# Kernel tuning notes

Measured on AMD Instinct MI355X. Metric: run time of the kernel, lower is better.

Reference implementation:

```python
import jax, jax.numpy as jnp
import numpy as np

DIM_TIME = 100
NUM_HEAD = 8
DIM_OUT = 256
LN_EPS = 1e-5

# fixed (non-trainable) TimeEncode frequencies: 1 / 10**linspace(0, 9, dim)
_TIME_W = jnp.asarray((1.0 / 10 ** np.linspace(0, 9, DIM_TIME, dtype=np.float32)))


def setup_inputs() -> dict:
    key = jax.random.key(0)
    ks = jax.random.split(key, 16)
    D, E, S = 25000, 500000, 525000
    dn, de = 128, 128
    def lin(k, out_d, in_d):
        return jax.random.normal(k, (out_d, in_d), jnp.float32) * (1.0 / np.sqrt(in_d))
    return {
        "h": jax.random.normal(ks[0], (S, dn), jnp.float32),
        "f": jax.random.normal(ks[1], (E, de), jnp.float32),
        "dt": jax.random.uniform(ks[2], (E,), jnp.float32) * 1000.0,
        "Wq_lin": lin(ks[3], DIM_OUT, dn + DIM_TIME),
        "bq_lin": jnp.zeros((DIM_OUT,), jnp.float32),
        "Wkv_lin": lin(ks[4], DIM_OUT, dn + de + DIM_TIME),
        "bkv_lin": jnp.zeros((DIM_OUT,), jnp.float32),
        "Wq": lin(ks[5], DIM_OUT, DIM_OUT),
        "bq": jnp.zeros((DIM_OUT,), jnp.float32),
        "Wk": lin(ks[6], DIM_OUT, DIM_OUT),
        "bk": jnp.zeros((DIM_OUT,), jnp.float32),
        "Wv": lin(ks[7], DIM_OUT, DIM_OUT),
        "bv": jnp.zeros((DIM_OUT,), jnp.float32),
        "ln_g": jnp.ones((DIM_OUT,), jnp.float32),
        "ln_b": jnp.zeros((DIM_OUT,), jnp.float32),
        "dst": jax.random.randint(ks[8], (E,), 0, D, jnp.int64 if jax.config.jax_enable_x64 else jnp.int32),
    }


def reference(h, f, dt, Wq_lin, bq_lin, Wkv_lin, bkv_lin, Wq, bq, Wk, bk, Wv, bv, ln_g, ln_b, dst):
    E = dst.shape[0]
    D = h.shape[0] - E          # num_dst_nodes; src node D+i is the source of edge i
    H = NUM_HEAD
    dh = DIM_OUT // H

    # TimeEncode (frozen, no grad in original): cos(w * t + 0)
    time_feat = jax.lax.stop_gradient(jnp.cos(dt[:, None] * _TIME_W[None, :]))      # [E, Dt]
    zero_time_feat = jnp.ones((D, DIM_TIME), h.dtype)                               # cos(0) = 1

    # Q from dst nodes; K/V from src-neighbor nodes + edge feat + time feat
    Q_ori = jnp.concatenate([h[:D], zero_time_feat], axis=1) @ Wq_lin.T + bq_lin    # [D, dout]
    K_ori = jnp.concatenate([h[D:], f, time_feat], axis=1) @ Wkv_lin.T + bkv_lin    # [E, dout]

    # augmented edge set: E real edges + D self-loops (dst attends to itself)
    Qfull = jnp.concatenate([Q_ori[dst], Q_ori], axis=0)                            # [E+D, dout]
    KVfull = jnp.concatenate([K_ori, Q_ori], axis=0)                                # [E+D, dout]

    Qh = (Qfull @ Wq.T + bq).reshape(-1, H, dh)
    Kh = (KVfull @ Wk.T + bk).reshape(-1, H, dh)
    Vh = (KVfull @ Wv.T + bv).reshape(-1, H, dh)

    scores = jax.nn.leaky_relu(jnp.sum(Qh * Kh, axis=2), negative_slope=0.2)        # [E+D, H]

    dst_all = jnp.concatenate([dst, jnp.arange(D, dtype=dst.dtype)], axis=0)        # [E+D]

    # segment (edge) softmax over destination nodes; every dst has a self-loop
    seg_max = jnp.full((D, H), -jnp.inf, scores.dtype).at[dst_all].max(scores)
    ex = jnp.exp(scores - seg_max[dst_all])
    seg_sum = jnp.zeros((D, H), scores.dtype).at[dst_all].add(ex)
    att = ex / seg_sum[dst_all]                                                     # [E+D, H]

    # weighted scatter-sum aggregation (copy_u/sum over the augmented block)
    Vw = (Vh * att[:, :, None]).reshape(-1, DIM_OUT)                                # [E+D, dout]
    agg = jnp.zeros((D, DIM_OUT), h.dtype).at[dst_all].add(Vw)                      # [D, dout]

    rst = jax.nn.relu(agg)                                                          # dropout = identity (eval)
    mu = jnp.mean(rst, axis=-1, keepdims=True)
    var = jnp.mean((rst - mu) ** 2, axis=-1, keepdims=True)
    return (rst - mu) * jax.lax.rsqrt(var + LN_EPS) * ln_g + ln_b
```

## Files before the change

kernel.cpp:

```cpp
#include <hip/hip_runtime.h>
#include <cstdint>
#include <cstddef>


typedef _Float16 f16_t;
typedef _Float16 f16x8 __attribute__((ext_vector_type(8)));
typedef _Float16 f16x4 __attribute__((ext_vector_type(4)));
typedef float    f32x4 __attribute__((ext_vector_type(4)));

#define MFMA16(a, b, c) __builtin_amdgcn_mfma_f32_16x16x32_f16(a, b, c, 0, 0, 0)

#define BARRIER()                                         \
  do {                                                    \
    asm volatile("s_waitcnt lgkmcnt(0)" ::: "memory");    \
    __builtin_amdgcn_sched_barrier(0);                    \
    __builtin_amdgcn_s_barrier();                         \
    __builtin_amdgcn_sched_barrier(0);                    \
  } while (0)

static __device__ __forceinline__ f32x4 zero4() {
  f32x4 v; v[0] = 0.f; v[1] = 0.f; v[2] = 0.f; v[3] = 0.f; return v;
}

#define TIMEW_LOG2 (-0.30199346317157837f)

__global__ void k_prep(const float* __restrict__ wq_lin,
                       const float* __restrict__ bq_lin,
                       const float* __restrict__ wq,
                       const float* __restrict__ wk,
                       const float* __restrict__ wv,
                       f16_t* __restrict__ wq1,
                       f16_t* __restrict__ w3,
                       float* __restrict__ bqe) {
  int i = blockIdx.x * 256 + threadIdx.x;
  if (i < 32768) {
    int o = i >> 7, k = i & 127;
    wq1[i] = (f16_t)wq_lin[o * 228 + k];
  } else if (i < 229376) {
    int j = i - 32768;
    int r = j >> 8, k = j & 255;
    const float* src = (r < 256) ? wq : ((r < 512) ? wk : wv);
    w3[j] = (f16_t)src[(r & 255) * 256 + k];
  } else if (i < 229632) {
    int o = i - 229376;
    float s = bq_lin[o];
    for (int j = 0; j < 100; ++j) s += wq_lin[o * 228 + 128 + j];
    bqe[o] = s;
  }
}

__global__ __launch_bounds__(384) void k_wcomp(
    const float* __restrict__ wkv_lin, const float* __restrict__ bkv,
    const float* __restrict__ wk, const float* __restrict__ bk,
    const float* __restrict__ wv, const float* __restrict__ bv,
    f16_t* __restrict__ weffp, float* __restrict__ beff) {
  __shared__ float wrow[256];
  const int oc = blockIdx.x;
  const float* src = (oc < 256) ? (wk + (size_t)oc * 256)
                                : (wv + (size_t)(oc - 256) * 256);
  const int t = threadIdx.x;
  if (t < 256) wrow[t] = src[t];
  __syncthreads();

  float acc = 0.f;
  if (t < 356) {
#pragma unroll 4
    for (int m = 0; m < 256; ++m) acc += wrow[m] * wkv_lin[(size_t)m * 356 + t];
  }
  int kc = t >> 5, g = (t >> 3) & 3, j = t & 7;
  weffp[(size_t)kc * 16384 + g * 4096 + oc * 8 + j] = (f16_t)acc;

  if (t == 0) {
    float b = (oc < 256) ? bk[oc] : bv[oc - 256];
    for (int m = 0; m < 256; ++m) b += wrow[m] * bkv[m];
    beff[oc] = b;
  }
}

__global__ void k_hist(const int* __restrict__ dst, int* __restrict__ rs, int E) {
  int e = blockIdx.x * 256 + threadIdx.x;
  if (e < E) atomicAdd(&rs[dst[e] + 1], 1);
}

__global__ void k_scan(int* __restrict__ rs, int* __restrict__ cur, int D) {
  __shared__ int sd[1024];
  __shared__ int srun;
  const int t = threadIdx.x;
  if (t == 0) srun = 0;
  __syncthreads();
  for (int base = 0; base < D; base += 1024) {
    const int i = base + t;
    int c = (i < D) ? rs[i + 1] : 0;
    sd[t] = c;
    __syncthreads();
    for (int off = 1; off < 1024; off <<= 1) {
      int v = (t >= off) ? sd[t - off] : 0;
      __syncthreads();
      sd[t] += v;
      __syncthreads();
    }
    const int incl = sd[t];
    const int run = srun;
    __syncthreads();
    if (i < D) {
      cur[i] = run + incl - c;
      rs[i + 1] = run + incl;
    }
    if (t == 1023) srun = run + sd[1023];
    __syncthreads();
  }
}

__global__ void k_scatter(const int* __restrict__ dst, int* __restrict__ cur,
                          int* __restrict__ csr, int* __restrict__ dstc, int E) {
  int e = blockIdx.x * 256 + threadIdx.x;
  if (e < E) {
    int d = dst[e];
    int pos = atomicAdd(&cur[d], 1);
    csr[pos] = e;
    dstc[pos] = d;
  }
}

__global__ void k_sentinel(float* __restrict__ o, int n) {
  int i = blockIdx.x * 256 + threadIdx.x;
  if (i < n) o[i] = 1e30f;
}

__global__ __launch_bounds__(512) void k_q(
    const float* __restrict__ h, const float* __restrict__ bqe,
    const float* __restrict__ bq, const float* __restrict__ bk,
    const float* __restrict__ bv, const f16_t* __restrict__ wq1,
    const f16_t* __restrict__ w3, float* __restrict__ qhd,
    f16_t* __restrict__ khs, f16_t* __restrict__ vhs, int D) {
  __shared__ f16_t sm[64 * 256];
  f16_t* xs = sm;
  f16_t* ks = sm;
  const int tid = threadIdx.x;
  const int dbase = blockIdx.x * 64;

  {
    const int r = tid >> 3, q = tid & 7;
    const int dd = min(dbase + r, D - 1);
    const int sw = r & 7;
    const float* p = h + (size_t)dd * 128 + q * 16;
#pragma unroll
    for (int u = 0; u < 2; ++u) {
      float4 v0 = *(const float4*)(p + u * 8);
      float4 v1 = *(const float4*)(p + u * 8 + 4);
      f16x8 w8;
      w8[0] = (f16_t)v0.x; w8[1] = (f16_t)v0.y; w8[2] = (f16_t)v0.z; w8[3] = (f16_t)v0.w;
      w8[4] = (f16_t)v1.x; w8[5] = (f16_t)v1.y; w8[6] = (f16_t)v1.z; w8[7] = (f16_t)v1.w;
      *(f16x8*)&xs[r * 128 + (((2 * q + u) ^ sw) << 3)] = w8;
    }
  }
  __syncthreads();

  const int lane = tid & 63;
  const int wv_ = tid >> 6;
  const int m16 = lane & 15;
  const int g = lane >> 4;

  f32x4 acc1[4][2];
#pragma unroll
  for (int mt = 0; mt < 4; ++mt)
#pragma unroll
    for (int nt = 0; nt < 2; ++nt) acc1[mt][nt] = zero4();

#pragma unroll
  for (int kt = 0; kt < 4; ++kt) {
    f16x8 a[4];
#pragma unroll
    for (int mt = 0; mt < 4; ++mt) {
      int row = mt * 16 + m16;
      a[mt] = *(const f16x8*)&xs[row * 128 + ((((kt << 2) + g) ^ (row & 7)) << 3)];
    }
#pragma unroll
    for (int nt = 0; nt < 2; ++nt) {
      int col = wv_ * 32 + nt * 16 + m16;
      f16x8 b = *(const f16x8*)&wq1[(size_t)col * 128 + (kt << 5) + (g << 3)];
#pragma unroll
      for (int mt = 0; mt < 4; ++mt) acc1[mt][nt] = MFMA16(a[mt], b, acc1[mt][nt]);
    }
  }
  __syncthreads();

#pragma unroll
  for (int nt = 0; nt < 2; ++nt) {
    int col = wv_ * 32 + nt * 16 + m16;
    float bias = bqe[col];
#pragma unroll
    for (int mt = 0; mt < 4; ++mt)
#pragma unroll
      for (int j = 0; j < 4; ++j) {
        int row = mt * 16 + (g << 2) + j;
        ks[row * 256 + ((((col >> 3) ^ (row & 7)) << 3)) + (col & 7)] =
            (f16_t)(acc1[mt][nt][j] + bias);
      }
  }
  __syncthreads();

#pragma unroll
  for (int p = 0; p < 3; ++p) {
    const f16_t* wsec = w3 + ((size_t)p << 16);
    const float* bsec = (p == 0) ? bq : ((p == 1) ? bk : bv);
    f32x4 acc[4][2];
#pragma unroll
    for (int mt = 0; mt < 4; ++mt)
#pragma unroll
      for (int nt = 0; nt < 2; ++nt) acc[mt][nt] = zero4();
#pragma unroll
    for (int kt = 0; kt < 8; ++kt) {
      f16x8 a[4];
#pragma unroll
      for (int mt = 0; mt < 4; ++mt) {
        int row = mt * 16 + m16;
        a[mt] = *(const f16x8*)&ks[row * 256 + ((((kt << 2) + g) ^ (row & 7)) << 3)];
      }
#pragma unroll
      for (int nt = 0; nt < 2; ++nt) {
        int col = wv_ * 32 + nt * 16 + m16;
        f16x8 b = *(const f16x8*)&wsec[(size_t)col * 256 + (kt << 5) + (g << 3)];
#pragma unroll
        for (int mt = 0; mt < 4; ++mt) acc[mt][nt] = MFMA16(a[mt], b, acc[mt][nt]);
      }
    }
#pragma unroll
    for (int nt = 0; nt < 2; ++nt) {
      int col = wv_ * 32 + nt * 16 + m16;
      float bias = bsec[col];
#pragma unroll
      for (int mt = 0; mt < 4; ++mt)
#pragma unroll
        for (int j = 0; j < 4; ++j) {
          int row = mt * 16 + (g << 2) + j;
          int dd = dbase + row;
          if (dd < D) {
            float val = acc[mt][nt][j] + bias;
            if (p == 0)
              qhd[(size_t)dd * 256 + col] = val;
            else if (p == 1)
              khs[(size_t)dd * 256 + col] = (f16_t)val;
            else
              vhs[(size_t)dd * 256 + col] = (f16_t)val;
          }
        }
    }
  }
}

__global__ __launch_bounds__(512, 4) void k_kv(
    const float* __restrict__ h, const float* __restrict__ f,
    const float* __restrict__ dt, const f16_t* __restrict__ weffp,
    const float* __restrict__ beff, const int* __restrict__ csr,
    const int* __restrict__ dstc, const float* __restrict__ qhd,
    float* __restrict__ agg, int D, int E) {
  __shared__ __align__(16) unsigned char smem[40960];

  const int tid = threadIdx.x;
  const int pbase = blockIdx.x * 64;
  const int row = tid >> 3, q = tid & 7;
  const int lane = tid & 63, wn = tid >> 6;
  const int m16 = lane & 15, g = lane >> 4;

  const int pclamp = min(pbase + row, E - 1);
  const int ec = csr[pclamp];
  const float dtv = dt[ec];
  const float* hrow = h + (size_t)(D + ec) * 128 + q * 4;
  const float* frow = f + (size_t)ec * 128 + q * 4;

  auto stageA = [&](int buf, int sub, float4 v) {
    f16x4 w;
    w[0] = (f16_t)v.x; w[1] = (f16_t)v.y; w[2] = (f16_t)v.z; w[3] = (f16_t)v.w;
    *(f16x4*)(smem + buf * 20480 + sub * 5120 + row * 80 + q * 8) = w;
  };
  const f16_t* wb = weffp + (size_t)g * 4096 + ((size_t)(wn * 64 + m16) << 3);
  auto gldB = [&](int kc, f16x8* d) {
    const f16_t* pB = wb + (size_t)kc * 16384;
#pragma unroll
    for (int n = 0; n < 4; ++n) d[n] = *(const f16x8*)(pB + n * 128);
  };

  f32x4 acc[4][4];
#pragma unroll
  for (int mt = 0; mt < 4; ++mt)
#pragma unroll
    for (int n = 0; n < 4; ++n) acc[mt][n] = zero4();

  auto doChunk = [&](int kc, const f16x8* bbuf) {
    const unsigned char* Ac =
        smem + (((kc >> 2) == 1) ? 20480 : 0) + (kc & 3) * 5120;
#pragma unroll
    for (int mt = 0; mt < 4; ++mt) {
      f16x8 afr = *(const f16x8*)(Ac + (mt * 16 + m16) * 80 + g * 16);
#pragma unroll
      for (int n = 0; n < 4; ++n) acc[mt][n] = MFMA16(afr, bbuf[n], acc[mt][n]);
    }
  };

  float4 hv[4], fv[4];
#pragma unroll
  for (int s = 0; s < 4; ++s) hv[s] = *(const float4*)(hrow + s * 32);
#pragma unroll
  for (int s = 0; s < 4; ++s) fv[s] = *(const float4*)(frow + s * 32);
#pragma unroll
  for (int s = 0; s < 4; ++s) stageA(0, s, hv[s]);
#pragma unroll
  for (int s = 0; s < 4; ++s) stageA(1, s, fv[s]);
  BARRIER();

  f16x8 bb0[4], bb1[4];
  gldB(0, bb0);
  gldB(1, bb1); doChunk(0, bb0);
  gldB(2, bb0); doChunk(1, bb1);
  gldB(3, bb1); doChunk(2, bb0);
  gldB(4, bb0); doChunk(3, bb1);
  BARRIER();

#pragma unroll
  for (int s = 0; s < 4; ++s) {
    float4 a;
#pragma unroll
    for (int j = 0; j < 4; ++j) {
      int cc = s * 32 + q * 4 + j;
      ((float*)&a)[j] =
          (cc < 100) ? __cosf(dtv * exp2f(TIMEW_LOG2 * (float)cc)) : 0.f;
    }
    stageA(0, s, a);
  }
  gldB(5, bb1); doChunk(4, bb0);
  gldB(6, bb0); doChunk(5, bb1);
  gldB(7, bb1); doChunk(6, bb0);
  gldB(8, bb0); doChunk(7, bb1);
  BARRIER();

  gldB(9, bb1);  doChunk(8, bb0);
  gldB(10, bb0); doChunk(9, bb1);
  gldB(11, bb1); doChunk(10, bb0);
  doChunk(11, bb1);
  BARRIER();

  f16_t* ep    = (f16_t*)smem;
  float* ee_s  = (float*)(smem + 33792);
  int*   dst_s = (int*)(smem + 35840);

  if (wn < 4) {
#pragma unroll
    for (int n = 0; n < 4; ++n) {
      const int c256 = wn * 64 + n * 16 + m16;
      const float bias = beff[c256];
#pragma unroll
      for (int mt = 0; mt < 4; ++mt)
#pragma unroll
        for (int j = 0; j < 4; ++j) {
          const int r2 = mt * 16 + (g << 2) + j;
          ep[r2 * 264 + c256] = (f16_t)(acc[mt][n][j] + bias);
        }
    }
  }
  BARRIER();

  {
    const int r2 = tid >> 3, hp = tid & 7;
    const int p2 = pbase + r2;
    float eev = 0.f;
    if (p2 < E) {
      const int de = dstc[p2];
      const float* qp = qhd + (size_t)de * 256 + hp * 32;
      const f16_t* kp = ep + r2 * 264 + hp * 32;
      float s = 0.f;
#pragma unroll
      for (int jj = 0; jj < 32; jj += 4) {
        float4 qv = *(const float4*)(qp + jj);
        f16x4 kv = *(const f16x4*)(kp + jj);
        s += qv.x * (float)kv[0] + qv.y * (float)kv[1] +
             qv.z * (float)kv[2] + qv.w * (float)kv[3];
      }
      s = (s > 0.f) ? s : 0.2f * s;
      eev = __expf(s);
    }
    ee_s[r2 * 8 + hp] = eev;
    if (hp == 0) dst_s[r2] = dstc[min(p2, E - 1)];
  }
  BARRIER();

  if (wn >= 4) {
#pragma unroll
    for (int n = 0; n < 4; ++n) {
      const int c256 = (wn - 4) * 64 + n * 16 + m16;
      const float bias = beff[256 + c256];
#pragma unroll
      for (int mt = 0; mt < 4; ++mt)
#pragma unroll
        for (int j = 0; j < 4; ++j) {
          const int r2 = mt * 16 + (g << 2) + j;
          ep[r2 * 264 + c256] = (f16_t)(acc[mt][n][j] + bias);
        }
    }
  }
  BARRIER();

  if (tid < 264) {
    const int c = tid;
    const int hd = (c < 256) ? (c >> 5) : (c - 256);
    float accv = 0.f;
    int cur_d = dst_s[0];
#pragma unroll 8
    for (int r = 0; r < 64; ++r) {
      int dd = dst_s[r];
      if (dd != cur_d) {
        atomicAdd(&agg[(size_t)cur_d * 264 + c], accv);
        accv = 0.f;
        cur_d = dd;
      }
      float eev = ee_s[r * 8 + hd];
      if (c < 256)
        accv = fmaf(eev, (float)ep[r * 264 + c], accv);
      else
        accv += eev;
    }
    atomicAdd(&agg[(size_t)cur_d * 264 + c], accv);
  }
}

__global__ __launch_bounds__(256) void k_fin(
    const float* __restrict__ qhd, const f16_t* __restrict__ khs,
    const f16_t* __restrict__ vhs, const float* __restrict__ agg,
    const float* __restrict__ lng, const float* __restrict__ lnb,
    float* __restrict__ out, int D) {
  const int lane = threadIdx.x & 63;
  const int d = blockIdx.x * 4 + (threadIdx.x >> 6);
  if (d >= D) return;
  const int c0 = lane * 4;
  const int hd = lane >> 3;

  float4 av = *(const float4*)(agg + (size_t)d * 264 + c0);
  float den = agg[(size_t)d * 264 + 256 + hd];

  {
    float4 qv = *(const float4*)(qhd + (size_t)d * 256 + c0);
    f16x4 ku = *(const f16x4*)(khs + (size_t)d * 256 + c0);
    f16x4 vu = *(const f16x4*)(vhs + (size_t)d * 256 + c0);
    float s = qv.x * (float)ku[0] + qv.y * (float)ku[1] +
              qv.z * (float)ku[2] + qv.w * (float)ku[3];
    s += __shfl_xor(s, 1); s += __shfl_xor(s, 2); s += __shfl_xor(s, 4);
    s = (s > 0.f) ? s : 0.2f * s;
    float ee = __expf(s);
    den += ee;
    av.x = fmaf(ee, (float)vu[0], av.x);
    av.y = fmaf(ee, (float)vu[1], av.y);
    av.z = fmaf(ee, (float)vu[2], av.z);
    av.w = fmaf(ee, (float)vu[3], av.w);
  }

  float x0 = fmaxf(av.x / den, 0.f), x1 = fmaxf(av.y / den, 0.f);
  float x2 = fmaxf(av.z / den, 0.f), x3 = fmaxf(av.w / den, 0.f);

  float s1 = x0 + x1 + x2 + x3;
#pragma unroll
  for (int m = 1; m < 64; m <<= 1) s1 += __shfl_xor(s1, m);
  float mu = s1 * (1.f / 256.f);
  float d0 = x0 - mu, d1 = x1 - mu, d2 = x2 - mu, d3 = x3 - mu;
  float s2 = d0 * d0 + d1 * d1 + d2 * d2 + d3 * d3;
#pragma unroll
  for (int m = 1; m < 64; m <<= 1) s2 += __shfl_xor(s2, m);
  float rstd = rsqrtf(s2 * (1.f / 256.f) + 1e-5f);

  float4 gg = *(const float4*)(lng + c0);
  float4 bb = *(const float4*)(lnb + c0);
  float4 o;
  o.x = d0 * rstd * gg.x + bb.x;
  o.y = d1 * rstd * gg.y + bb.y;
  o.z = d2 * rstd * gg.z + bb.z;
  o.w = d3 * rstd * gg.w + bb.w;
  *(float4*)(out + (size_t)d * 256 + c0) = o;
}

extern "C" void kernel_launch(void* const* d_in, const int* in_sizes, int n_in,
                              void* d_out, int out_size, void* d_ws,
                              size_t ws_size, hipStream_t stream) {
  const float* h       = (const float*)d_in[0];
  const float* f       = (const float*)d_in[1];
  const float* dt      = (const float*)d_in[2];
  const float* wq_lin  = (const float*)d_in[3];
  const float* bq_lin  = (const float*)d_in[4];
  const float* wkv_lin = (const float*)d_in[5];
  const float* bkv_lin = (const float*)d_in[6];
  const float* wq      = (const float*)d_in[7];
  const float* bq      = (const float*)d_in[8];
  const float* wk      = (const float*)d_in[9];
  const float* bk      = (const float*)d_in[10];
  const float* wv      = (const float*)d_in[11];
  const float* bv      = (const float*)d_in[12];
  const float* lng     = (const float*)d_in[13];
  const float* lnb     = (const float*)d_in[14];
  const int*   dst     = (const int*)d_in[15];

  const int S = in_sizes[0] / 128;
  const int E = in_sizes[2];
  const int D = S - E;
  float* out = (float*)d_out;

  char* p = (char*)d_ws;
  size_t off = 0;
  auto take = [&](size_t bytes) -> char* {
    char* r = p + off;
    off += (bytes + 255) & ~(size_t)255;
    return r;
  };
  f16_t* wq1   = (f16_t*)take((size_t)32768 * 2);
  f16_t* w3    = (f16_t*)take((size_t)196608 * 2);
  float* bqe   = (float*)take((size_t)256 * 4);
  f16_t* weffp = (f16_t*)take((size_t)196608 * 2);
  float* beff  = (float*)take((size_t)512 * 4);
  float* qhd   = (float*)take((size_t)D * 256 * 4);
  f16_t* khs   = (f16_t*)take((size_t)D * 256 * 2);
  f16_t* vhs   = (f16_t*)take((size_t)D * 256 * 2);
  float* agg   = (float*)take((size_t)D * 264 * 4);
  int*   rs    = (int*)  take((size_t)(D + 1) * 4);
  int*   cur   = (int*)  take((size_t)D * 4);
  int*   csr   = (int*)  take((size_t)E * 4);
  int*   dstc  = (int*)  take((size_t)E * 4);

  if (off > ws_size) {
    k_sentinel<<<(out_size + 255) / 256, 256, 0, stream>>>(out, out_size);
    return;
  }

  hipMemsetAsync(rs, 0, (size_t)(D + 1) * 4, stream);
  hipMemsetAsync(agg, 0, (size_t)D * 264 * 4, stream);
  k_prep<<<898, 256, 0, stream>>>(wq_lin, bq_lin, wq, wk, wv, wq1, w3, bqe);
  k_wcomp<<<512, 384, 0, stream>>>(wkv_lin, bkv_lin, wk, bk, wv, bv, weffp,
                                   beff);
  k_hist<<<(E + 255) / 256, 256, 0, stream>>>(dst, rs, E);
  k_scan<<<1, 1024, 0, stream>>>(rs, cur, D);
  k_scatter<<<(E + 255) / 256, 256, 0, stream>>>(dst, cur, csr, dstc, E);
  k_q<<<(D + 63) / 64, 512, 0, stream>>>(h, bqe, bq, bk, bv, wq1, w3, qhd, khs,
                                         vhs, D);
  k_kv<<<(E + 63) / 64, 512, 0, stream>>>(h, f, dt, weffp, beff, csr, dstc,
                                          qhd, agg, D, E);
  k_fin<<<(D + 3) / 4, 256, 0, stream>>>(qhd, khs, vhs, agg, lng, lnb, out, D);
}
```

Measured before the change: 596.9 us.

## Fuse small setup kernels, speed up scan, split scatter-reduce across all threads

```diff
diff --git a/kernel.cpp b/kernel.cpp
--- a/kernel.cpp
+++ b/kernel.cpp
@@ -24,15 +24,23 @@
 
 #define TIMEW_LOG2 (-0.30199346317157837f)
 
-__global__ void k_prep(const float* __restrict__ wq_lin,
-                       const float* __restrict__ bq_lin,
-                       const float* __restrict__ wq,
-                       const float* __restrict__ wk,
-                       const float* __restrict__ wv,
-                       f16_t* __restrict__ wq1,
-                       f16_t* __restrict__ w3,
-                       float* __restrict__ bqe) {
-  int i = blockIdx.x * 256 + threadIdx.x;
+__global__ void k_ph(const float* __restrict__ wq_lin,
+                     const float* __restrict__ bq_lin,
+                     const float* __restrict__ wq,
+                     const float* __restrict__ wk,
+                     const float* __restrict__ wv,
+                     const int* __restrict__ dst,
+                     f16_t* __restrict__ wq1,
+                     f16_t* __restrict__ w3,
+                     float* __restrict__ bqe,
+                     int* __restrict__ rs, int E) {
+  const int b = blockIdx.x;
+  if (b >= 898) {
+    int e = (b - 898) * 256 + threadIdx.x;
+    if (e < E) atomicAdd(&rs[dst[e] + 1], 1);
+    return;
+  }
+  int i = b * 256 + threadIdx.x;
   if (i < 32768) {
     int o = i >> 7, k = i & 127;
     wq1[i] = (f16_t)wq_lin[o * 228 + k];
@@ -77,48 +85,43 @@
   }
 }
 
-__global__ void k_hist(const int* __restrict__ dst, int* __restrict__ rs, int E) {
-  int e = blockIdx.x * 256 + threadIdx.x;
-  if (e < E) atomicAdd(&rs[dst[e] + 1], 1);
-}
-
-__global__ void k_scan(int* __restrict__ rs, int* __restrict__ cur, int D) {
-  __shared__ int sd[1024];
+__global__ __launch_bounds__(1024) void k_scan(int* __restrict__ rs,
+                                               int* __restrict__ cur, int D) {
+  __shared__ int wsum[16];
   __shared__ int srun;
-  const int t = threadIdx.x;
+  const int t = threadIdx.x, lane = t & 63, wv = t >> 6;
   if (t == 0) srun = 0;
   __syncthreads();
   for (int base = 0; base < D; base += 1024) {
     const int i = base + t;
-    int c = (i < D) ? rs[i + 1] : 0;
-    sd[t] = c;
+    const int c = (i < D) ? rs[i + 1] : 0;
+    int x = c;
+#pragma unroll
+    for (int off = 1; off < 64; off <<= 1) {
+      int y = __shfl_up(x, off);
+      if (lane >= off) x += y;
+    }
+    if (lane == 63) wsum[wv] = x;
     __syncthreads();
-    for (int off = 1; off < 1024; off <<= 1) {
-      int v = (t >= off) ? sd[t - off] : 0;
-      __syncthreads();
-      sd[t] += v;
-      __syncthreads();
-    }
-    const int incl = sd[t];
+    if (wv == 0 && lane < 16) {
+      int w = wsum[lane];
+#pragma unroll
+      for (int off = 1; off < 16; off <<= 1) {
+        int y = __shfl_up(w, off);
+        if (lane >= off) w += y;
+      }
+      wsum[lane] = w;
+    }
+    __syncthreads();
+    const int incl = x + ((wv > 0) ? wsum[wv - 1] : 0);
     const int run = srun;
     __syncthreads();
     if (i < D) {
       cur[i] = run + incl - c;
       rs[i + 1] = run + incl;
     }
-    if (t == 1023) srun = run + sd[1023];
+    if (t == 1023) srun = run + incl;
     __syncthreads();
-  }
-}
-
-__global__ void k_scatter(const int* __restrict__ dst, int* __restrict__ cur,
-                          int* __restrict__ csr, int* __restrict__ dstc, int E) {
-  int e = blockIdx.x * 256 + threadIdx.x;
-  if (e < E) {
-    int d = dst[e];
-    int pos = atomicAdd(&cur[d], 1);
-    csr[pos] = e;
-    dstc[pos] = d;
   }
 }
 
@@ -127,13 +130,25 @@
   if (i < n) o[i] = 1e30f;
 }
 
-__global__ __launch_bounds__(512) void k_q(
+__global__ __launch_bounds__(512) void k_sq(
     const float* __restrict__ h, const float* __restrict__ bqe,
     const float* __restrict__ bq, const float* __restrict__ bk,
     const float* __restrict__ bv, const f16_t* __restrict__ wq1,
     const f16_t* __restrict__ w3, float* __restrict__ qhd,
-    f16_t* __restrict__ khs, f16_t* __restrict__ vhs, int D) {
+    f16_t* __restrict__ khs, f16_t* __restrict__ vhs, int D,
+    const int* __restrict__ dst, int* __restrict__ cur,
+    int* __restrict__ csr, int* __restrict__ dstc, int E, int nq) {
   __shared__ f16_t sm[64 * 256];
+  if ((int)blockIdx.x >= nq) {
+    int e = ((int)blockIdx.x - nq) * 512 + (int)threadIdx.x;
+    if (e < E) {
+      int d = dst[e];
+      int pos = atomicAdd(&cur[d], 1);
+      csr[pos] = e;
+      dstc[pos] = d;
+    }
+    return;
+  }
   f16_t* xs = sm;
   f16_t* ks = sm;
   const int tid = threadIdx.x;
@@ -303,18 +318,19 @@
   for (int s = 0; s < 4; ++s) hv[s] = *(const float4*)(hrow + s * 32);
 #pragma unroll
   for (int s = 0; s < 4; ++s) fv[s] = *(const float4*)(frow + s * 32);
-#pragma unroll
-  for (int s = 0; s < 4; ++s) stageA(0, s, hv[s]);
-#pragma unroll
-  for (int s = 0; s < 4; ++s) stageA(1, s, fv[s]);
-  BARRIER();
-
   f16x8 bb0[4], bb1[4];
   gldB(0, bb0);
-  gldB(1, bb1); doChunk(0, bb0);
-  gldB(2, bb0); doChunk(1, bb1);
-  gldB(3, bb1); doChunk(2, bb0);
-  gldB(4, bb0); doChunk(3, bb1);
+  gldB(1, bb1);
+#pragma unroll
+  for (int s = 0; s < 4; ++s) stageA(0, s, hv[s]);
+#pragma unroll
+  for (int s = 0; s < 4; ++s) stageA(1, s, fv[s]);
+  BARRIER();
+
+  doChunk(0, bb0); gldB(2, bb0);
+  doChunk(1, bb1); gldB(3, bb1);
+  doChunk(2, bb0); gldB(4, bb0);
+  doChunk(3, bb1);
   BARRIER();
 
 #pragma unroll
@@ -400,26 +416,41 @@
   }
   BARRIER();
 
-  if (tid < 264) {
-    const int c = tid;
-    const int hd = (c < 256) ? (c >> 5) : (c - 256);
+  {
+    const int half = tid >> 8;
+    const int c = tid & 255;
+    const int hd = c >> 5;
+    const int r0 = half * 32;
     float accv = 0.f;
-    int cur_d = dst_s[0];
+    int cur_d = dst_s[r0];
 #pragma unroll 8
-    for (int r = 0; r < 64; ++r) {
+    for (int r = r0; r < r0 + 32; ++r) {
       int dd = dst_s[r];
       if (dd != cur_d) {
         atomicAdd(&agg[(size_t)cur_d * 264 + c], accv);
         accv = 0.f;
         cur_d = dd;
       }
-      float eev = ee_s[r * 8 + hd];
-      if (c < 256)
-        accv = fmaf(eev, (float)ep[r * 264 + c], accv);
-      else
-        accv += eev;
+      accv = fmaf(ee_s[r * 8 + hd], (float)ep[r * 264 + c], accv);
     }
     atomicAdd(&agg[(size_t)cur_d * 264 + c], accv);
+  }
+  if (tid < 16) {
+    const int half = tid >> 3, hd = tid & 7;
+    const int r0 = half * 32;
+    float accv = 0.f;
+    int cur_d = dst_s[r0];
+#pragma unroll 8
+    for (int r = r0; r < r0 + 32; ++r) {
+      int dd = dst_s[r];
+      if (dd != cur_d) {
+        atomicAdd(&agg[(size_t)cur_d * 264 + 256 + hd], accv);
+        accv = 0.f;
+        cur_d = dd;
+      }
+      accv += ee_s[r * 8 + hd];
+    }
+    atomicAdd(&agg[(size_t)cur_d * 264 + 256 + hd], accv);
   }
 }
 
@@ -527,16 +558,18 @@
     return;
   }
 
-  hipMemsetAsync(rs, 0, (size_t)(D + 1) * 4, stream);
-  hipMemsetAsync(agg, 0, (size_t)D * 264 * 4, stream);
-  k_prep<<<898, 256, 0, stream>>>(wq_lin, bq_lin, wq, wk, wv, wq1, w3, bqe);
+  const int nq = (D + 63) / 64;
+  const int nsc = (E + 511) / 512;
+
+  hipMemsetAsync(agg, 0, (size_t)((char*)rs - (char*)agg) + (size_t)(D + 1) * 4,
+                 stream);
+  k_ph<<<898 + (E + 255) / 256, 256, 0, stream>>>(wq_lin, bq_lin, wq, wk, wv,
+                                                  dst, wq1, w3, bqe, rs, E);
   k_wcomp<<<512, 384, 0, stream>>>(wkv_lin, bkv_lin, wk, bk, wv, bv, weffp,
                                    beff);
-  k_hist<<<(E + 255) / 256, 256, 0, stream>>>(dst, rs, E);
   k_scan<<<1, 1024, 0, stream>>>(rs, cur, D);
-  k_scatter<<<(E + 255) / 256, 256, 0, stream>>>(dst, cur, csr, dstc, E);
-  k_q<<<(D + 63) / 64, 512, 0, stream>>>(h, bqe, bq, bk, bv, wq1, w3, qhd, khs,
-                                         vhs, D);
+  k_sq<<<nq + nsc, 512, 0, stream>>>(h, bqe, bq, bk, bv, wq1, w3, qhd, khs,
+                                     vhs, D, dst, cur, csr, dstc, E, nq);
   k_kv<<<(E + 63) / 64, 512, 0, stream>>>(h, f, dt, weffp, beff, csr, dstc,
                                           qhd, agg, D, E);
   k_fin<<<(D + 3) / 4, 256, 0, stream>>>(qhd, khs, vhs, agg, lng, lnb, out, D);
```

Measured after the change: 503.7 us. 15.6% less time.
